# Kernel optimization log

Hardware: AMD Instinct MI355X
Metric: run time of the kernel (lower is better)

Reference implementation:

```python
import jax, jax.numpy as jnp
import numpy as np

N_GAUSSIANS = 512
N_PIXELS = 262144  # 512x512 image


def setup_inputs() -> dict:
    key = jax.random.key(0)
    k1, k2, k3, k4, k5 = jax.random.split(key, 5)
    x = jax.random.uniform(k1, (N_PIXELS, 2), dtype=jnp.float32)
    alphas = (1.0 / N_GAUSSIANS) ** 0.5 * jax.random.uniform(k2, (N_GAUSSIANS, 1), dtype=jnp.float32)
    means = jax.random.uniform(k3, (N_GAUSSIANS, 2), dtype=jnp.float32)
    rotations = jnp.pi * jax.random.uniform(k4, (N_GAUSSIANS, 1), dtype=jnp.float32)
    scales = 0.1 * jax.random.uniform(k5, (N_GAUSSIANS, 2), dtype=jnp.float32)
    return {"x": x, "alphas": alphas, "means": means, "rotations": rotations, "scales": scales}


def _inv2x2(m):
    # m: [N, 2, 2] -> elementwise 2x2 inverse
    a, b = m[:, 0, 0], m[:, 0, 1]
    c, d = m[:, 1, 0], m[:, 1, 1]
    det = a * d - b * c
    inv = jnp.stack([jnp.stack([d, -b], axis=-1),
                     jnp.stack([-c, a], axis=-1)], axis=-2)
    return inv / det[:, None, None]


def reference(x, alphas, means, rotations, scales):
    rot = rotations[:, 0]                       # [N]
    cth, sth = jnp.cos(rot), jnp.sin(rot)
    s0, s1 = scales[:, 0], scales[:, 1]
    # RS = R @ diag(s): [N, 2, 2]
    RS = jnp.stack([s0 * cth, -s1 * sth, s0 * sth, s1 * cth], axis=-1).reshape(-1, 2, 2)
    RSSR = jnp.einsum('nij,nkj->nik', RS, RS)   # RS @ RS^T
    cov = _inv2x2(RSSR)                          # [N, 2, 2]
    rel = x[:, None, :] - means[None, :, :]      # [P, N, 2]
    q = jnp.einsum('pni,nij,pnj->pn', rel, cov, rel)  # quadratic form [P, N]
    g = jnp.exp(-q / 2)                          # [P, N]
    return g @ alphas                            # [P, 1]
```

## Files before the change

kernel.cpp:

```cpp
#include <hip/hip_runtime.h>

#define NG 512
#define NPX 262144
#define BLOCK 256
#define GTILE 4
#define PPT 2
#define HALFPX (NPX / 2)

#if __has_builtin(__builtin_amdgcn_exp2f)
  #define KSCALE 0.72134752044448170368f
  #define EXPNEG(w) __builtin_amdgcn_exp2f(-(w))
#else
  #define KSCALE 0.5f
  #define EXPNEG(w) __expf(-(w))
#endif

__global__ void gsplat_prep(const float* __restrict__ alphas,
                            const float* __restrict__ means,
                            const float* __restrict__ rotations,
                            const float* __restrict__ scales,
                            float4* __restrict__ ga,
                            float2* __restrict__ gb)
{
    int n = blockIdx.x * blockDim.x + threadIdx.x;
    if (n >= NG) return;

    float rot = rotations[n];
    float sth, cth;
    sincosf(rot, &sth, &cth);
    float s0 = scales[2 * n + 0];
    float s1 = scales[2 * n + 1];
    float r00 = s0 * cth, r01 = -s1 * sth;
    float r10 = s0 * sth, r11 =  s1 * cth;
    float Ar = r00 * r00 + r01 * r01;
    float Br = r00 * r10 + r01 * r11;
    float Dr = r10 * r10 + r11 * r11;
    float det = Ar * Dr - Br * Br;
    float kc00 =  KSCALE * Dr / det;
    float kc01 = -KSCALE * Br / det;
    float p00 = sqrtf(kc00);
    float p01 = kc01 / p00;
    float p11 = sqrtf(KSCALE / Dr);
    float mx = means[2 * n + 0];
    float my = means[2 * n + 1];
    float nuoff = -(p00 * mx + p01 * my);
    float nvoff = -(p11 * my);

    ga[n] = make_float4(p00, p01, nuoff, alphas[n]);
    gb[n] = make_float2(p11, nvoff);
}

__global__ __launch_bounds__(BLOCK)
void gsplat_main(const float* __restrict__ x,
                 const float4* __restrict__ ga,
                 const float2* __restrict__ gb,
                 float* __restrict__ out)
{
    int tid = blockIdx.x * BLOCK + threadIdx.x;
    float2 pv0 = ((const float2*)x)[tid];
    float2 pv1 = ((const float2*)x)[tid + HALFPX];
    float x0 = pv0.x, y0 = pv0.y;
    float x1 = pv1.x, y1 = pv1.y;

    float accA0 = 0.0f, accA1 = 0.0f;
    float accB0 = 0.0f, accB1 = 0.0f;

    float4 ca[GTILE]; float2 cb[GTILE];
    float4 na[GTILE]; float2 nb[GTILE];

    #pragma unroll
    for (int j = 0; j < GTILE; ++j) { ca[j] = ga[j]; cb[j] = gb[j]; }

    #define COMPUTE_TILE(A, B)                                                \
        _Pragma("unroll")                                                     \
        for (int j = 0; j < GTILE; ++j) {                                     \
            float czu = A[j].z;              \
            float czv = B[j].y;                                               \
            float u0 = fmaf(A[j].x, x0, fmaf(A[j].y, y0, czu));               \
            float v0 = fmaf(B[j].x, y0, czv);                                 \
            float w0 = fmaf(v0, v0, u0 * u0);                                 \
            float e0 = EXPNEG(w0);                                            \
            float u1 = fmaf(A[j].x, x1, fmaf(A[j].y, y1, czu));               \
            float v1 = fmaf(B[j].x, y1, czv);                                 \
            float w1 = fmaf(v1, v1, u1 * u1);                                 \
            float e1 = EXPNEG(w1);                                            \
            if (j & 1) { accA1 = fmaf(A[j].w, e0, accA1);                     \
                         accB1 = fmaf(A[j].w, e1, accB1); }                   \
            else       { accA0 = fmaf(A[j].w, e0, accA0);                     \
                         accB0 = fmaf(A[j].w, e1, accB0); }                   \
        }

    for (int t = 0; t < NG; t += 2 * GTILE) {
        #pragma unroll
        for (int j = 0; j < GTILE; ++j) {
            int n = (t + GTILE + j) & (NG - 1);
            na[j] = ga[n]; nb[j] = gb[n];
        }
        COMPUTE_TILE(ca, cb)

        #pragma unroll
        for (int j = 0; j < GTILE; ++j) {
            int n = (t + 2 * GTILE + j) & (NG - 1);
            ca[j] = ga[n]; cb[j] = gb[n];
        }
        COMPUTE_TILE(na, nb)
    }
    #undef COMPUTE_TILE

    out[tid]          = accA0 + accA1;
    out[tid + HALFPX] = accB0 + accB1;
}

extern "C" void kernel_launch(void* const* d_in, const int* in_sizes, int n_in,
                              void* d_out, int out_size, void* d_ws, size_t ws_size,
                              hipStream_t stream) {
    const float* x         = (const float*)d_in[0];
    const float* alphas    = (const float*)d_in[1];
    const float* means     = (const float*)d_in[2];
    const float* rotations = (const float*)d_in[3];
    const float* scales    = (const float*)d_in[4];
    float* out = (float*)d_out;

    float4* ga = (float4*)d_ws;
    float2* gb = (float2*)((char*)d_ws + NG * 16);

    gsplat_prep<<<(NG + 255) / 256, 256, 0, stream>>>(alphas, means, rotations, scales, ga, gb);

    int grid = NPX / (BLOCK * PPT);
    gsplat_main<<<grid, BLOCK, 0, stream>>>(x, ga, gb, out);
}
```

Measured before the change: 99.63 us.

## Split gaussian loop across four blocks per pixel tile with atomic accumulation

Each pixel tile is now processed by four blocks, each summing over a quarter of the gaussians, and partial sums are combined with atomicAdd into the output. The prep kernel is enlarged to also zero the output buffer. This quadruples the grid to raise occupancy and latency hiding on a GPU that previously had only about two blocks per CU. In exchange it adds global atomics, an extra output zeroing pass, and redundant pixel loads per block.

```diff
diff --git a/kernel.cpp b/kernel.cpp
--- a/kernel.cpp
+++ b/kernel.cpp
@@ -5,6 +5,8 @@
 #define BLOCK 256
 #define GTILE 4
 #define PPT 2
+#define GSPLIT 4
+#define GPB (NG / GSPLIT)
 #define HALFPX (NPX / 2)
 
 #if __has_builtin(__builtin_amdgcn_exp2f)
@@ -20,10 +22,13 @@
                             const float* __restrict__ rotations,
                             const float* __restrict__ scales,
                             float4* __restrict__ ga,
-                            float2* __restrict__ gb)
+                            float2* __restrict__ gb,
+                            float* __restrict__ out)
 {
-    int n = blockIdx.x * blockDim.x + threadIdx.x;
-    if (n >= NG) return;
+    int t = blockIdx.x * blockDim.x + threadIdx.x;
+    out[t] = 0.0f;
+    if (t >= NG) return;
+    int n = t;
 
     float rot = rotations[n];
     float sth, cth;
@@ -56,7 +61,11 @@
                  const float2* __restrict__ gb,
                  float* __restrict__ out)
 {
-    int tid = blockIdx.x * BLOCK + threadIdx.x;
+    int bid = blockIdx.x;
+    int pixblk = bid >> 2;
+    int gbase  = (bid & 3) * GPB;
+
+    int tid = pixblk * BLOCK + threadIdx.x;
     float2 pv0 = ((const float2*)x)[tid];
     float2 pv1 = ((const float2*)x)[tid + HALFPX];
     float x0 = pv0.x, y0 = pv0.y;
@@ -69,7 +78,7 @@
     float4 na[GTILE]; float2 nb[GTILE];
 
     #pragma unroll
-    for (int j = 0; j < GTILE; ++j) { ca[j] = ga[j]; cb[j] = gb[j]; }
+    for (int j = 0; j < GTILE; ++j) { ca[j] = ga[gbase + j]; cb[j] = gb[gbase + j]; }
 
     #define COMPUTE_TILE(A, B)                                                \
         _Pragma("unroll")                                                     \
@@ -90,25 +99,25 @@
                          accB0 = fmaf(A[j].w, e1, accB0); }                   \
         }
 
-    for (int t = 0; t < NG; t += 2 * GTILE) {
+    for (int t = 0; t < GPB; t += 2 * GTILE) {
         #pragma unroll
         for (int j = 0; j < GTILE; ++j) {
-            int n = (t + GTILE + j) & (NG - 1);
+            int n = gbase + ((t + GTILE + j) & (GPB - 1));
             na[j] = ga[n]; nb[j] = gb[n];
         }
         COMPUTE_TILE(ca, cb)
 
         #pragma unroll
         for (int j = 0; j < GTILE; ++j) {
-            int n = (t + 2 * GTILE + j) & (NG - 1);
+            int n = gbase + ((t + 2 * GTILE + j) & (GPB - 1));
             ca[j] = ga[n]; cb[j] = gb[n];
         }
         COMPUTE_TILE(na, nb)
     }
     #undef COMPUTE_TILE
 
-    out[tid]          = accA0 + accA1;
-    out[tid + HALFPX] = accB0 + accB1;
+    atomicAdd(&out[tid],          accA0 + accA1);
+    atomicAdd(&out[tid + HALFPX], accB0 + accB1);
 }
 
 extern "C" void kernel_launch(void* const* d_in, const int* in_sizes, int n_in,
@@ -124,8 +133,8 @@
     float4* ga = (float4*)d_ws;
     float2* gb = (float2*)((char*)d_ws + NG * 16);
 
-    gsplat_prep<<<(NG + 255) / 256, 256, 0, stream>>>(alphas, means, rotations, scales, ga, gb);
+    gsplat_prep<<<NPX / BLOCK, BLOCK, 0, stream>>>(alphas, means, rotations, scales, ga, gb, out);
 
-    int grid = NPX / (BLOCK * PPT);
+    int grid = (NPX / (BLOCK * PPT)) * GSPLIT;
     gsplat_main<<<grid, BLOCK, 0, stream>>>(x, ga, gb, out);
 }
```

Measured after the change: 89.80 us. 9.9% less time.
